# Kernel tuning notes

Hardware: AMD Instinct MI355X
Metric: run time of the kernel (lower is better)

The kernel has to match this reference:

```python
import jax, jax.numpy as jnp
import numpy as np

DIM = 512
HEADS = 8
DIM_HEAD = 64
INNER = HEADS * DIM_HEAD  # 512
PATCH = 64
M = 3
IN_CH = PATCH * PATCH // 2      # 2048
OUT_CH = IN_CH // 2             # 1024
B, N = 8, PATCH * PATCH // 4    # 8, 1024
SCALE = DIM_HEAD ** -0.5


def setup_inputs() -> dict:
    key = jax.random.key(0)
    ks = jax.random.split(key, 16)
    rn = lambda k, shp, s: (jax.random.normal(k, shp, dtype=jnp.float32) * s)
    inp = rn(ks[0], (B, N, DIM), 1.0)
    x = rn(ks[1], (B, N, DIM), 1.0)
    y = rn(ks[2], (B, N, DIM), 1.0)
    # Linear params (torch convention: W [out, in], y = x @ W.T + b)
    Wq = rn(ks[3], (INNER, DIM), DIM ** -0.5)
    bq = jnp.zeros((INNER,), jnp.float32)
    Wkv = rn(ks[4], (2 * INNER, DIM), DIM ** -0.5)
    bkv = jnp.zeros((2 * INNER,), jnp.float32)
    Wf = rn(ks[5], (OUT_CH + M, IN_CH + M), (IN_CH + M) ** -0.5)
    bf = jnp.zeros((OUT_CH + M,), jnp.float32)
    Wo = rn(ks[6], (DIM, INNER), INNER ** -0.5)
    bo = jnp.zeros((DIM,), jnp.float32)
    # memory tokens (xavier_normal std = sqrt(2/(m+inner)))
    std = np.sqrt(2.0 / (M + INNER))
    m_k = rn(ks[7], (1, M, INNER), std)
    m_v = rn(ks[8], (1, M, INNER), std)
    Sm_k = rn(ks[9], (1, M, INNER), std)
    Sm_v = rn(ks[10], (1, M, INNER), std)
    return dict(inp=inp, x=x, y=y, Wq=Wq, bq=bq, Wkv=Wkv, bkv=bkv,
                Wf=Wf, bf=bf, Wo=Wo, bo=bo,
                m_k=m_k, m_v=m_v, Sm_k=Sm_k, Sm_v=Sm_v)


def _split_heads(t):
    # 'b n (h d) -> b h n d'
    b, n, _ = t.shape
    return t.reshape(b, n, HEADS, DIM_HEAD).transpose(0, 2, 1, 3)


def _mem_view(p, b):
    # torch: p.expand(b, M, INNER).view(b, HEADS, M, DIM_HEAD) — raw reshape
    return jnp.broadcast_to(p, (b, M, INNER)).reshape(b, HEADS, M, DIM_HEAD)


def reference(inp, x, y, Wq, bq, Wkv, bkv, Wf, bf, Wo, bo, m_k, m_v, Sm_k, Sm_v):
    b = inp.shape[0]
    context = jnp.concatenate([x, y], axis=1)            # [b, 2n, dim]
    q = _split_heads(inp @ Wq.T + bq)                    # [b, h, n, d]
    kv = context @ Wkv.T + bkv
    k, v = jnp.split(kv, 2, axis=-1)
    k, v = _split_heads(k), _split_heads(v)              # [b, h, 2n, d]
    mk = np.sqrt(DIM_HEAD).astype(np.float32) * _mem_view(m_k, b)
    mv = np.sqrt(M).astype(np.float32) * _mem_view(m_v, b)
    k = jnp.concatenate([k, mk], axis=2)                 # [b, h, 2n+m, d]
    v = jnp.concatenate([v, mv], axis=2)
    dots = jnp.einsum('bhid,bhjd->bhij', q, k) * SCALE
    cross_attn = jax.nn.softmax(dots, axis=-1)           # [b, h, n, 2n+m]

    skv = inp @ Wkv.T + bkv
    S_k, S_v = jnp.split(skv, 2, axis=-1)
    S_k, S_v = _split_heads(S_k), _split_heads(S_v)      # [b, h, n, d]
    Smk = np.sqrt(DIM_HEAD).astype(np.float32) * _mem_view(Sm_k, b)
    Smv = np.sqrt(M).astype(np.float32) * _mem_view(Sm_v, b)
    Sk = jnp.concatenate([S_k, Smk], axis=2)             # [b, h, n+m, d]
    Sv = jnp.concatenate([S_v, Smv], axis=2)
    dots2 = jnp.einsum('bhid,bhjd->bhij', q, Sk) * SCALE
    self_attn = jax.nn.softmax(dots2, axis=-1)           # [b, h, n, n+m]

    cross_attn = cross_attn @ Wf.T + bf                  # [b, h, n, n+m]
    attn = cross_attn + self_attn
    out = jnp.einsum('bhij,bhjd->bhid', attn, Sv)        # [b, h, n, d]
    out = out.transpose(0, 2, 1, 3).reshape(b, -1, INNER)
    return out @ Wo.T + bo                               # [b, n, dim]
```

## Files before the change

### kernel.cpp

```cpp
#include <hip/hip_runtime.h>
#include <hip/hip_bf16.h>
#include <type_traits>

using bf16 = __hip_bfloat16;
typedef float f32x4 __attribute__((ext_vector_type(4)));
typedef __bf16 bf16x8_t __attribute__((ext_vector_type(8)));
typedef short  s16x8_t  __attribute__((ext_vector_type(8)));

template <typename V, typename = void> struct MfmaWorks : std::false_type {};
template <typename V>
struct MfmaWorks<V, std::void_t<decltype(__builtin_amdgcn_mfma_f32_16x16x32_bf16(
    std::declval<V>(), std::declval<V>(), std::declval<f32x4>(), 0, 0, 0))>> : std::true_type {};
using frag_t = std::conditional_t<MfmaWorks<bf16x8_t>::value, bf16x8_t, s16x8_t>;

template <typename V>
__device__ __forceinline__ f32x4 mfma_16x16x32(V a, V b, f32x4 c) {
    return __builtin_amdgcn_mfma_f32_16x16x32_bf16(a, b, c, 0, 0, 0);
}

__device__ __forceinline__ void gld_lds16(const void* g, void* l) {
    __builtin_amdgcn_global_load_lds(
        (const __attribute__((address_space(1))) unsigned int*)g,
        (__attribute__((address_space(3))) unsigned int*)l, 16, 0, 0);
}

__device__ __forceinline__ unsigned pack2(float lo, float hi) {
    bf16 a = __float2bfloat16(lo), b = __float2bfloat16(hi);
    unsigned short al, bl;
    __builtin_memcpy(&al, &a, 2);
    __builtin_memcpy(&bl, &b, 2);
    return (unsigned)al | ((unsigned)bl << 16);
}

__device__ __forceinline__ float ldin(const void* p, long i, int f32) {
    return f32 ? ((const float*)p)[i] : __bfloat162float(((const bf16*)p)[i]);
}

__device__ __forceinline__ int detect_f32(const void* __restrict__ inp) {
    __shared__ int sflag;
    const int t = threadIdx.x;
    if (t < 64) {
        int cnt = 0;
#pragma unroll
        for (int s = 0; s < 4; s++) {
            float v = __bfloat162float(((const bf16*)inp)[2 * (t + 64 * s)]);
            float a = fabsf(v);
            bool sane = (a == 0.f) || (a > 9e-4f && a < 1000.f);
            unsigned long long m = __ballot(sane);
            cnt += (int)__popcll(m);
        }
        if (t == 0) sflag = (cnt > 128) ? 0 : 1;
    }
    __syncthreads();
    return sflag;
}

__global__ __launch_bounds__(256)
void prep_all(const void* __restrict__ inp, const void* __restrict__ x,
              const void* __restrict__ y,
              const void* __restrict__ Wq, const void* __restrict__ Wkv,
              const void* __restrict__ Wo, const void* __restrict__ Wf,
              const void* __restrict__ bff, const void* __restrict__ bq,
              const void* __restrict__ bkv, const void* __restrict__ bo,
              const void* __restrict__ mk, const void* __restrict__ Smk,
              const void* __restrict__ Smv,
              bf16* __restrict__ inpB, bf16* __restrict__ ctxB,
              bf16* __restrict__ WqB, bf16* __restrict__ WkvB, bf16* __restrict__ WoB,
              bf16* __restrict__ WfT, bf16* __restrict__ bqB, bf16* __restrict__ bkvB,
              bf16* __restrict__ boB, bf16* __restrict__ kb, bf16* __restrict__ Skb,
              bf16* __restrict__ GTS, bf16* __restrict__ SvC, float qscale)
{
    const int f = detect_f32(inp);
    const int blk = blockIdx.x;
    const int t = threadIdx.x;
    const float SQRT3 = 1.7320508f;

    if (blk < 2048) {
        const long i0 = ((long)blk * 256 + t) * 8;
#pragma unroll
        for (int u = 0; u < 8; u++)
            inpB[i0 + u] = __float2bfloat16(ldin(inp, i0 + u, f));
    } else if (blk < 6144) {
        const long i0 = ((long)(blk - 2048) * 256 + t) * 8;
        const long r = i0 >> 9, c0 = i0 & 511;
        const long b = r >> 11, jj = r & 2047;
        const void* src = (jj < 1024) ? x : y;
        const long  soff = (jj < 1024) ? ((b * 1024 + jj) * 512 + c0)
                                       : ((b * 1024 + (jj - 1024)) * 512 + c0);
#pragma unroll
        for (int u = 0; u < 8; u++)
            ctxB[i0 + u] = __float2bfloat16(ldin(src, soff + u, f));
    } else if (blk < 6656) {
        const int wb = blk - 6144;
        long id = (long)wb * 256 + t;
        const void* src; bf16* dst; float sc;
        if (wb < 128)      { src = Wq;  dst = WqB;  sc = qscale; }
        else if (wb < 384) { src = Wkv; dst = WkvB; sc = 1.f; id -= 128L * 256; }
        else               { src = Wo;  dst = WoB;  sc = 1.f; id -= 384L * 256; }
        const long i0 = id * 8;
#pragma unroll
        for (int u = 0; u < 8; u++)
            dst[i0 + u] = __float2bfloat16(sc * ldin(src, i0 + u, f));
    } else if (blk < 7778) {
        const long i0 = ((long)(blk - 6656) * 256 + t) * 8;
        if (i0 >= 2176L * 1056) return;
        const long j = i0 / 1056, r0 = i0 % 1056;
        __align__(16) bf16 tmp[8];
#pragma unroll
        for (int u = 0; u < 8; u++) {
            const long r = r0 + u;
            float v = 0.f;
            if (r < 1027) {
                if (j < 2051)       v = ldin(Wf, r * 2051 + j, f);
                else if (j == 2051) v = ldin(bff, r, f);
            }
            tmp[u] = __float2bfloat16(v);
        }
        *(uint4*)(WfT + i0) = *(const uint4*)tmp;
    } else if (blk < 7781) {
        const void* src; bf16* dst; int n; float sc;
        switch (blk - 7778) {
            case 0:  src = bq;  dst = bqB;  n = 512;  sc = qscale; break;
            case 1:  src = bkv; dst = bkvB; n = 1024; sc = 1.f;    break;
            default: src = bo;  dst = boB;  n = 512;  sc = 1.f;    break;
        }
        for (int i = t; i < n; i += 256)
            dst[i] = __float2bfloat16(sc * ldin(src, i, f));
    } else if (blk < 8037) {
        const long e = ((long)(blk - 7781) * 256 + t) * 8;
        const long bh = e >> 13, rem = e & 8191;
        const long jj = rem >> 6, dg0 = rem & 63;
        const long h = bh & 7;
        __align__(16) bf16 tmp[8];
#pragma unroll
        for (int u = 0; u < 8; u++) {
            float v = (jj < 3) ? 8.f * ldin(mk, jj * 512 + h * 64 + dg0 + u, f) : 0.f;
            tmp[u] = __float2bfloat16(v);
        }
        *(uint4*)(kb + (bh * 2176 + 2048 + jj) * 64 + dg0) = *(const uint4*)tmp;
    } else if (blk < 8293) {
        const long e = ((long)(blk - 8037) * 256 + t) * 8;
        const long bh = e >> 13, rem = e & 8191;
        const long jj = rem >> 6, dg0 = rem & 63;
        const long h = bh & 7;
        __align__(16) bf16 tmp[8];
#pragma unroll
        for (int u = 0; u < 8; u++) {
            float v = (jj < 3) ? 8.f * ldin(Smk, jj * 512 + h * 64 + dg0 + u, f) : 0.f;
            tmp[u] = __float2bfloat16(v);
        }
        *(uint4*)(Skb + (bh * 1152 + 1024 + jj) * 64 + dg0) = *(const uint4*)tmp;
    } else {
        const long e = ((long)(blk - 8293) * 256 + t) * 8;
        const long bh = e >> 11, rem = e & 2047;
        const long dd = rem >> 5, jc0 = rem & 31;
        const long h = bh & 7;
        __align__(16) bf16 tmp[8];
#pragma unroll
        for (int u = 0; u < 8; u++) {
            const long jc = jc0 + u;
            float v = (jc < 3) ? SQRT3 * ldin(Smv, jc * 512 + h * 64 + dd, f) : 0.f;
            tmp[u] = __float2bfloat16(v);
        }
        *(uint4*)(GTS + (bh * 128 + dd) * 3136 + 3104 + jc0) = *(const uint4*)tmp;
        *(uint4*)(SvC + (bh * 64 + dd) * 1056 + 1024 + jc0)  = *(const uint4*)tmp;
    }
}

#define BK 32

__global__ __launch_bounds__(256)
void gemm_qkv(const bf16* __restrict__ A, const bf16* __restrict__ B,
              const bf16* __restrict__ bias,
              bf16* __restrict__ qb, bf16* __restrict__ Skb,
              bf16* __restrict__ GTS, bf16* __restrict__ SvC)
{
    __shared__ __align__(16) short As[128 * BK];
    __shared__ __align__(16) short Bs[128 * BK];

    const int t = threadIdx.x;
    const int wave = t >> 6, lane = t & 63;
    const int bn = blockIdx.x, bm = blockIdx.y;

    const bf16* Ab = A + (long)bm * 128 * 512;
    const bf16* Bb = B + (long)bn * 128 * 512;

    const int lrow = t >> 2, lcol = (t & 3) << 3;

    const f32x4 vzero = {0.f, 0.f, 0.f, 0.f};
    f32x4 acc[4][4];
#pragma unroll
    for (int i = 0; i < 4; i++)
#pragma unroll
        for (int j = 0; j < 4; j++) acc[i][j] = vzero;

    const int wr = (wave >> 1) << 6;
    const int wc = (wave & 1) << 6;
    const int fr = lane & 15;
    const int fq = (lane >> 4) << 3;

    for (int k0 = 0; k0 < 512; k0 += BK) {
        __syncthreads();
        gld_lds16(Ab + (long)lrow * 512 + (k0 + lcol),        (char*)As + wave * 1024);
        gld_lds16(Ab + (long)(64 + lrow) * 512 + (k0 + lcol), (char*)As + 4096 + wave * 1024);
        gld_lds16(Bb + (long)lrow * 512 + (k0 + lcol),        (char*)Bs + wave * 1024);
        gld_lds16(Bb + (long)(64 + lrow) * 512 + (k0 + lcol), (char*)Bs + 4096 + wave * 1024);
        __builtin_amdgcn_s_waitcnt(0);
        __syncthreads();

        frag_t af[4], bfr[4];
#pragma unroll
        for (int i = 0; i < 4; i++) af[i]  = *(const frag_t*)&As[(wr + i * 16 + fr) * BK + fq];
#pragma unroll
        for (int j = 0; j < 4; j++) bfr[j] = *(const frag_t*)&Bs[(wc + j * 16 + fr) * BK + fq];
#pragma unroll
        for (int i = 0; i < 4; i++)
#pragma unroll
            for (int j = 0; j < 4; j++)
                acc[i][j] = mfma_16x16x32<frag_t>(af[i], bfr[j], acc[i][j]);
    }

    const int r0 = bm * 128 + wr + ((lane >> 4) << 2);
    const int c0 = bn * 128 + wc + fr;
    const int bb = bm >> 3;
#pragma unroll
    for (int j = 0; j < 4; j++) {
        const int c = c0 + j * 16;
        const float bv = __bfloat162float(bias[c]);
        if (c < 512) {
#pragma unroll
            for (int i = 0; i < 4; i++)
#pragma unroll
                for (int r = 0; r < 4; r++) {
                    const long rg = r0 + i * 16 + r;
                    qb[rg * 512 + c] = __float2bfloat16(acc[i][j][r] + bv);
                }
        } else if (c < 1024) {
            const int h = (c - 512) >> 6, dg = c & 63;
            bf16* base = Skb + ((long)(bb * 8 + h) * 1152) * 64 + dg;
#pragma unroll
            for (int i = 0; i < 4; i++)
#pragma unroll
                for (int r = 0; r < 4; r++) {
                    const long jj = (r0 + i * 16 + r) & 1023;
                    base[jj * 64] = __float2bfloat16(acc[i][j][r] + bv);
                }
        } else {
            const int h = (c - 1024) >> 6, dd = c & 63;
            bf16* svt = GTS + ((long)(bb * 8 + h) * 128 + dd) * 3136 + 2080;
            bf16* svc = SvC + ((long)(bb * 8 + h) * 64 + dd) * 1056;
#pragma unroll
            for (int i = 0; i < 4; i++) {
                const long j0 = (r0 + i * 16) & 1023;
                __align__(8) bf16 t4[4];
#pragma unroll
                for (int r = 0; r < 4; r++) t4[r] = __float2bfloat16(acc[i][j][r] + bv);
                *(uint2*)(svt + j0) = *(const uint2*)t4;
                *(uint2*)(svc + j0) = *(const uint2*)t4;
            }
        }
    }
}

__global__ __launch_bounds__(256)
void gemm_gtck(const bf16* __restrict__ WfT, const bf16* __restrict__ SvC,
               bf16* __restrict__ GTS,
               const bf16* __restrict__ ctxB, const bf16* __restrict__ WkvB,
               const bf16* __restrict__ bkvB, bf16* __restrict__ kb)
{
    __shared__ __align__(16) short As[128 * BK];
    __shared__ __align__(16) short Bs[128 * BK];

    const int t = threadIdx.x;
    const int wave = t >> 6, lane = t & 63;
    const int id = blockIdx.x;
    const bool isGT = id < 544;

    int bn, bm, K;
    const bf16 *A, *B;
    long lda, ldb;
    if (isGT) { bn = id & 31; bm = id >> 5; A = WfT; lda = 1056; B = SvC; ldb = 1056; K = 1056; }
    else { const int i2 = id - 544; bn = i2 & 3; bm = i2 >> 2; A = ctxB; lda = 512; B = WkvB; ldb = 512; K = 512; }

    const bf16* Ab = A + (long)bm * 128 * lda;
    const bf16* Bb = B + (long)bn * 128 * ldb;

    const int lrow = t >> 2, lcol = (t & 3) << 3;

    const f32x4 vzero = {0.f, 0.f, 0.f, 0.f};
    f32x4 acc[4][4];
#pragma unroll
    for (int i = 0; i < 4; i++)
#pragma unroll
        for (int j = 0; j < 4; j++) acc[i][j] = vzero;

    const int wr = (wave >> 1) << 6;
    const int wc = (wave & 1) << 6;
    const int fr = lane & 15;
    const int fq = (lane >> 4) << 3;

    for (int k0 = 0; k0 < K; k0 += BK) {
        __syncthreads();
        gld_lds16(Ab + (long)lrow * lda + (k0 + lcol),        (char*)As + wave * 1024);
        gld_lds16(Ab + (long)(64 + lrow) * lda + (k0 + lcol), (char*)As + 4096 + wave * 1024);
        gld_lds16(Bb + (long)lrow * ldb + (k0 + lcol),        (char*)Bs + wave * 1024);
        gld_lds16(Bb + (long)(64 + lrow) * ldb + (k0 + lcol), (char*)Bs + 4096 + wave * 1024);
        __builtin_amdgcn_s_waitcnt(0);
        __syncthreads();

        frag_t af[4], bfr[4];
#pragma unroll
        for (int i = 0; i < 4; i++) af[i]  = *(const frag_t*)&As[(wr + i * 16 + fr) * BK + fq];
#pragma unroll
        for (int j = 0; j < 4; j++) bfr[j] = *(const frag_t*)&Bs[(wc + j * 16 + fr) * BK + fq];
#pragma unroll
        for (int i = 0; i < 4; i++)
#pragma unroll
            for (int j = 0; j < 4; j++)
                acc[i][j] = mfma_16x16x32<frag_t>(af[i], bfr[j], acc[i][j]);
    }

    const int r0 = bm * 128 + wr + ((lane >> 4) << 2);
    const int c0 = bn * 128 + wc + fr;

    if (isGT) {
#pragma unroll
        for (int j = 0; j < 4; j++) {
            const int c = c0 + j * 16;
            bf16* rowp = GTS + ((long)(c >> 6) * 128 + (c & 63)) * 3136;
#pragma unroll
            for (int i = 0; i < 4; i++) {
                const int rgb = r0 + i * 16;
                if (rgb >= 2080) continue;
                __align__(8) bf16 t4[4];
#pragma unroll
                for (int r = 0; r < 4; r++) t4[r] = __float2bfloat16(acc[i][j][r]);
                *(uint2*)(rowp + rgb) = *(const uint2*)t4;
            }
        }
    } else {
        const int bb = bm >> 4;
#pragma unroll
        for (int j = 0; j < 4; j++) {
            const int c = c0 + j * 16;
            const float bv = __bfloat162float(bkvB[c]);
            const int h = c >> 6, dg = c & 63;
            bf16* base = kb + ((long)(bb * 8 + h) * 2176) * 64 + dg;
#pragma unroll
            for (int i = 0; i < 4; i++)
#pragma unroll
                for (int r = 0; r < 4; r++) {
                    const long jj = (r0 + i * 16 + r) & 2047;
                    base[jj * 64] = __float2bfloat16(acc[i][j][r] + bv);
                }
        }
    }
}

__global__ __launch_bounds__(256)
void gemm_final64(const float* __restrict__ o0, const float* __restrict__ o1,
                  const bf16* __restrict__ B, const bf16* __restrict__ bias,
                  float* __restrict__ out)
{
    __shared__ __align__(16) short As[64 * BK];
    __shared__ __align__(16) short Bs[128 * BK];

    const int t = threadIdx.x;
    const int wave = t >> 6, lane = t & 63;
    const int bn = blockIdx.x, bm = blockIdx.y;

    const bf16* Bb = B + (long)bn * 128 * 512;
    const int lrow = t >> 2, lcol = (t & 3) << 3;

    const f32x4 vzero = {0.f, 0.f, 0.f, 0.f};
    f32x4 acc[2][4];
#pragma unroll
    for (int i = 0; i < 2; i++)
#pragma unroll
        for (int j = 0; j < 4; j++) acc[i][j] = vzero;

    const int wr = (wave >> 1) << 5;
    const int wc = (wave & 1) << 6;
    const int fr = lane & 15;
    const int fq = (lane >> 4) << 3;

    for (int k0 = 0; k0 < 512; k0 += BK) {
        __syncthreads();
        {
            const int ar = t >> 2, ac = (t & 3) << 3;
            const float* a0 = o0 + (long)(bm * 64 + ar) * 512 + k0 + ac;
            const float* a1 = o1 + (long)(bm * 64 + ar) * 512 + k0 + ac;
            __align__(16) bf16 tt[8];
#pragma unroll
            for (int u = 0; u < 2; u++) {
                const float4 v0 = *(const float4*)(a0 + u * 4);
                const float4 v1 = *(const float4*)(a1 + u * 4);
                tt[u * 4 + 0] = __float2bfloat16(v0.x + v1.x);
                tt[u * 4 + 1] = __float2bfloat16(v0.y + v1.y);
                tt[u * 4 + 2] = __float2bfloat16(v0.z + v1.z);
                tt[u * 4 + 3] = __float2bfloat16(v0.w + v1.w);
            }
            *(uint4*)&As[ar * BK + ac] = *(const uint4*)tt;
        }
        gld_lds16(Bb + (long)lrow * 512 + (k0 + lcol),        (char*)Bs + wave * 1024);
        gld_lds16(Bb + (long)(64 + lrow) * 512 + (k0 + lcol), (char*)Bs + 4096 + wave * 1024);
        __builtin_amdgcn_s_waitcnt(0);
        __syncthreads();

        frag_t af[2], bfr[4];
#pragma unroll
        for (int i = 0; i < 2; i++) af[i]  = *(const frag_t*)&As[(wr + i * 16 + fr) * BK + fq];
#pragma unroll
        for (int j = 0; j < 4; j++) bfr[j] = *(const frag_t*)&Bs[(wc + j * 16 + fr) * BK + fq];
#pragma unroll
        for (int i = 0; i < 2; i++)
#pragma unroll
            for (int j = 0; j < 4; j++)
                acc[i][j] = mfma_16x16x32<frag_t>(af[i], bfr[j], acc[i][j]);
    }

    const int r0 = bm * 64 + wr + ((lane >> 4) << 2);
    const int c0 = bn * 128 + wc + fr;
#pragma unroll
    for (int j = 0; j < 4; j++) {
        const int c = c0 + j * 16;
        const float bv = __bfloat162float(bias[c]);
#pragma unroll
        for (int i = 0; i < 2; i++)
#pragma unroll
            for (int r = 0; r < 4; r++) {
                const long rg = r0 + i * 16 + r;
                out[rg * 512 + c] = acc[i][j][r] + bv;
            }
    }
}

__global__ __launch_bounds__(256, 4)
void attn_fused(const bf16* __restrict__ q,
                const bf16* __restrict__ kb,
                const bf16* __restrict__ Skb,
                const bf16* __restrict__ GTS,
                float* __restrict__ out0,
                float* __restrict__ out1)
{
    __shared__ __align__(16) bf16 Ks[2][64 * 64];
    __shared__ __align__(16) bf16 Gs[2][64 * 64];
    __shared__ __align__(16) unsigned Psw[4][16][32];

    const int t = threadIdx.x;
    const int w = t >> 6, lane = t & 63;
    const int bh = blockIdx.x, bm = blockIdx.y;
    const int phase = blockIdx.z;
    const int b = bh >> 3, h = bh & 7;
    const int g  = lane >> 4;
    const int fr = lane & 15;

    const bf16* Qg = q + ((long)(b * 1024 + bm * 128)) * 512 + h * 64;
    {
        const int qr = t >> 3, qc0 = (t & 7) << 3;
#pragma unroll
        for (int u = 0; u < 4; u++)
            gld_lds16(Qg + (long)(u * 32 + qr) * 512 + qc0, (char*)Ks + u * 4096 + w * 1024);
    }
    __builtin_amdgcn_s_waitcnt(0);
    __syncthreads();

    frag_t qf[2][2];
#pragma unroll
    for (int it = 0; it < 2; it++)
#pragma unroll
        for (int kh = 0; kh < 2; kh++)
            qf[it][kh] = *(const frag_t*)&((const bf16*)Ks)[(w * 32 + it * 16 + fr) * 64 + kh * 32 + g * 8];
    __syncthreads();

    union { frag_t f; short s[8]; } ou;
#pragma unroll
    for (int i = 0; i < 8; i++) ou.s[i] = 0x3F80;
    const frag_t onesf = ou.f;

    const f32x4 vzero = {0.f, 0.f, 0.f, 0.f};
    const int rs = t >> 3, gs = t & 7;
    const int glo = gs ^ (rs & 7);

    const bf16* Kb = phase ? Skb + (long)bh * 1152 * 64 : kb + (long)bh * 2176 * 64;
    const bf16* Gb = GTS + (long)bh * 128 * 3136 + (phase ? 2080 : 0);
    const int NC = phase ? 17 : 33;
    const int valid = phase ? 1027 : 2051;

    f32x4 oacc[2][4];
    f32x4 lacc[2];
#pragma unroll
    for (int it = 0; it < 2; it++) {
        lacc[it] = vzero;
#pragma unroll
        for (int dt = 0; dt < 4; dt++) oacc[it][dt] = vzero;
    }

    gld_lds16(Kb + (long)rs * 64 + glo * 8,          (char*)Ks[0] + w * 1024);
    gld_lds16(Kb + (long)(32 + rs) * 64 + glo * 8,   (char*)Ks[0] + 4096 + w * 1024);
    gld_lds16(Gb + (long)rs * 3136 + glo * 8,        (char*)Gs[0] + w * 1024);
    gld_lds16(Gb + (long)(32 + rs) * 3136 + glo * 8, (char*)Gs[0] + 4096 + w * 1024);

    unsigned* prow = &Psw[w][fr][0];
    const int swzk = (fr & 7) << 2;

    for (int c = 0; c < NC; c++) {
        const int buf = c & 1;
        __builtin_amdgcn_s_waitcnt(0);
        __syncthreads();
        if (c + 1 < NC) {
            const bf16* Kc = Kb + (long)(c + 1) * 64 * 64;
            const bf16* Gc = Gb + (c + 1) * 64;
            gld_lds16(Kc + (long)rs * 64 + glo * 8,          (char*)Ks[buf ^ 1] + w * 1024);
            gld_lds16(Kc + (long)(32 + rs) * 64 + glo * 8,   (char*)Ks[buf ^ 1] + 4096 + w * 1024);
            gld_lds16(Gc + (long)rs * 3136 + glo * 8,        (char*)Gs[buf ^ 1] + w * 1024);
            gld_lds16(Gc + (long)(32 + rs) * 3136 + glo * 8, (char*)Gs[buf ^ 1] + 4096 + w * 1024);
        }
        const bf16* Kl = Ks[buf];
        const bf16* Gl = Gs[buf];

        f32x4 s2[2][4];
#pragma unroll
        for (int it = 0; it < 2; it++)
#pragma unroll
            for (int ct = 0; ct < 4; ct++) s2[it][ct] = vzero;
        __builtin_amdgcn_s_setprio(1);
#pragma unroll
        for (int ct = 0; ct < 4; ct++)
#pragma unroll
            for (int kh = 0; kh < 2; kh++) {
                const int gph = (kh * 4 + g) ^ (fr & 7);
                const frag_t kf = *(const frag_t*)&Kl[(ct * 16 + fr) * 64 + gph * 8];
                s2[0][ct] = mfma_16x16x32<frag_t>(kf, qf[0][kh], s2[0][ct]);
                s2[1][ct] = mfma_16x16x32<frag_t>(kf, qf[1][kh], s2[1][ct]);
            }
        __builtin_amdgcn_s_setprio(0);

        if (c == NC - 1) {
#pragma unroll
            for (int ct = 0; ct < 4; ct++)
#pragma unroll
                for (int r = 0; r < 4; r++) {
                    const int kAbs = c * 64 + ct * 16 + 4 * g + r;
                    if (kAbs >= valid) { s2[0][ct][r] = -1.0e30f; s2[1][ct][r] = -1.0e30f; }
                }
        }

        frag_t pa[2][2];
#pragma unroll
        for (int it = 0; it < 2; it++) {
#pragma unroll
            for (int ct = 0; ct < 4; ct++) {
                const unsigned w0 = pack2(exp2f(s2[it][ct][0]), exp2f(s2[it][ct][1]));
                const unsigned w1 = pack2(exp2f(s2[it][ct][2]), exp2f(s2[it][ct][3]));
                *(uint2*)&prow[(ct * 8 + 2 * g) ^ swzk] = make_uint2(w0, w1);
            }
#pragma unroll
            for (int kh = 0; kh < 2; kh++)
                pa[it][kh] = *(const frag_t*)&prow[(kh * 16 + 4 * g) ^ swzk];
        }

        __builtin_amdgcn_s_setprio(1);
#pragma unroll
        for (int kh = 0; kh < 2; kh++) {
            lacc[0] = mfma_16x16x32<frag_t>(pa[0][kh], onesf, lacc[0]);
            lacc[1] = mfma_16x16x32<frag_t>(pa[1][kh], onesf, lacc[1]);
#pragma unroll
            for (int dt = 0; dt < 4; dt++) {
                const int gph = (kh * 4 + g) ^ (fr & 7);
                const frag_t gf = *(const frag_t*)&Gl[(dt * 16 + fr) * 64 + gph * 8];
                oacc[0][dt] = mfma_16x16x32<frag_t>(pa[0][kh], gf, oacc[0][dt]);
                oacc[1][dt] = mfma_16x16x32<frag_t>(pa[1][kh], gf, oacc[1][dt]);
            }
        }
        __builtin_amdgcn_s_setprio(0);
    }

    float gba[4] = {0.f, 0.f, 0.f, 0.f};
    if (phase == 0) {
        const bf16* gp = GTS + (long)bh * 128 * 3136 + 2051;
#pragma unroll
        for (int dt = 0; dt < 4; dt++)
            gba[dt] = __bfloat162float(gp[(long)(dt * 16 + fr) * 3136]);
    }
    float* Og = (phase ? out1 : out0) + ((long)(b * 1024 + bm * 128)) * 512 + h * 64;
#pragma unroll
    for (int it = 0; it < 2; it++)
#pragma unroll
        for (int r = 0; r < 4; r++) {
            const float inv = 1.f / lacc[it][r];
#pragma unroll
            for (int dt = 0; dt < 4; dt++) {
                Og[(long)(w * 32 + it * 16 + g * 4 + r) * 512 + dt * 16 + fr] =
                    oacc[it][dt][r] * inv + gba[dt];
            }
        }
}

extern "C" void kernel_launch(void* const* d_in, const int* in_sizes, int n_in,
                              void* d_out, int out_size, void* d_ws, size_t ws_size,
                              hipStream_t stream)
{
    const void* inp  = d_in[0];
    const void* x    = d_in[1];
    const void* y    = d_in[2];
    const void* Wq   = d_in[3];
    const void* bq   = d_in[4];
    const void* Wkv  = d_in[5];
    const void* bkv  = d_in[6];
    const void* Wf   = d_in[7];
    const void* bff  = d_in[8];
    const void* Wo   = d_in[9];
    const void* bo   = d_in[10];
    const void* m_k  = d_in[11];
    const void* Sm_k = d_in[13];
    const void* Sm_v = d_in[14];

    char* ws = (char*)d_ws;
    bf16* WqB  = (bf16*)(ws + 256);
    bf16* WkvB = (bf16*)(ws + 524544);
    bf16* WoB  = (bf16*)(ws + 1573120);
    bf16* WfT  = (bf16*)(ws + 2097408);
    bf16* bqB  = (bf16*)(ws + 6693120);
    bf16* bkvB = (bf16*)(ws + 6694144);
    bf16* boB  = (bf16*)(ws + 6696192);
    bf16* qb   = (bf16*)(ws + 6706432);
    bf16* kb   = (bf16*)(ws + 15095040);
    bf16* Skb  = (bf16*)(ws + 32920832);
    bf16* GTS  = (bf16*)(ws + 42358016);
    char* OV   = ws + 93738240;

    bf16*  inpB  = (bf16*)(OV);
    bf16*  SvC   = (bf16*)(OV + 16777216);
    bf16*  ctxB  = (bf16*)(OV + 33554432);
    float* out0f = (float*)(OV);
    float* out1f = (float*)(OV + 16777216);

    const dim3 blk(256);
    const float QS = 0.125f * 1.44269504f;

    prep_all<<<dim3(8357), blk, 0, stream>>>(inp, x, y, Wq, Wkv, Wo, Wf, bff,
                                             bq, bkv, bo, m_k, Sm_k, Sm_v,
                                             inpB, ctxB, WqB, WkvB, WoB, WfT,
                                             bqB, bkvB, boB, kb, Skb, GTS, SvC, QS);

    gemm_qkv<<<dim3(12, 64), blk, 0, stream>>>(inpB, WqB, bqB, qb, Skb, GTS, SvC);

    gemm_gtck<<<dim3(1056), blk, 0, stream>>>(WfT, SvC, GTS, ctxB, WkvB, bkvB, kb);

    attn_fused<<<dim3(64, 8, 2), blk, 0, stream>>>(qb, kb, Skb, GTS, out0f, out1f);

    gemm_final64<<<dim3(4, 128), blk, 0, stream>>>(out0f, out1f, WoB, boB, (float*)d_out);
}
```

Before: 360.9 us.

## Halve GEMM M-tiles and split cross-attention key range to balance attention blocks

The two projection GEMMs now use 64-row tiles instead of 128, doubling the block count so more blocks run at once. The attention kernel previously gave 33 key chunks to the cross phase and 17 to the self phase, which left the two halves of the grid unevenly loaded. The cross range is now split at chunk 25, and the z=1 blocks process the cross tail plus the whole self phase. The two partial cross results are stored unnormalized with their row sums, and the final GEMM combines them and normalizes while loading. This costs an extra fp32 output buffer and row-sum buffers to read in the final GEMM, and less reuse per GEMM tile.

After: 389.0 us. 1.08x slower.

```diff
diff --git a/kernel.cpp b/kernel.cpp
--- a/kernel.cpp
+++ b/kernel.cpp
@@ -175,26 +175,25 @@
               bf16* __restrict__ qb, bf16* __restrict__ Skb,
               bf16* __restrict__ GTS, bf16* __restrict__ SvC)
 {
-    __shared__ __align__(16) short As[128 * BK];
+    __shared__ __align__(16) short As[64 * BK];
     __shared__ __align__(16) short Bs[128 * BK];
 
     const int t = threadIdx.x;
     const int wave = t >> 6, lane = t & 63;
     const int bn = blockIdx.x, bm = blockIdx.y;
 
-    const bf16* Ab = A + (long)bm * 128 * 512;
+    const bf16* Ab = A + (long)bm * 64 * 512;
     const bf16* Bb = B + (long)bn * 128 * 512;
-
     const int lrow = t >> 2, lcol = (t & 3) << 3;
 
     const f32x4 vzero = {0.f, 0.f, 0.f, 0.f};
-    f32x4 acc[4][4];
-#pragma unroll
-    for (int i = 0; i < 4; i++)
+    f32x4 acc[2][4];
+#pragma unroll
+    for (int i = 0; i < 2; i++)
 #pragma unroll
         for (int j = 0; j < 4; j++) acc[i][j] = vzero;
 
-    const int wr = (wave >> 1) << 6;
+    const int wr = (wave >> 1) << 5;
     const int wc = (wave & 1) << 6;
     const int fr = lane & 15;
     const int fq = (lane >> 4) << 3;
@@ -202,34 +201,33 @@
     for (int k0 = 0; k0 < 512; k0 += BK) {
         __syncthreads();
         gld_lds16(Ab + (long)lrow * 512 + (k0 + lcol),        (char*)As + wave * 1024);
-        gld_lds16(Ab + (long)(64 + lrow) * 512 + (k0 + lcol), (char*)As + 4096 + wave * 1024);
         gld_lds16(Bb + (long)lrow * 512 + (k0 + lcol),        (char*)Bs + wave * 1024);
         gld_lds16(Bb + (long)(64 + lrow) * 512 + (k0 + lcol), (char*)Bs + 4096 + wave * 1024);
         __builtin_amdgcn_s_waitcnt(0);
         __syncthreads();
 
-        frag_t af[4], bfr[4];
-#pragma unroll
-        for (int i = 0; i < 4; i++) af[i]  = *(const frag_t*)&As[(wr + i * 16 + fr) * BK + fq];
+        frag_t af[2], bfr[4];
+#pragma unroll
+        for (int i = 0; i < 2; i++) af[i]  = *(const frag_t*)&As[(wr + i * 16 + fr) * BK + fq];
 #pragma unroll
         for (int j = 0; j < 4; j++) bfr[j] = *(const frag_t*)&Bs[(wc + j * 16 + fr) * BK + fq];
 #pragma unroll
-        for (int i = 0; i < 4; i++)
+        for (int i = 0; i < 2; i++)
 #pragma unroll
             for (int j = 0; j < 4; j++)
                 acc[i][j] = mfma_16x16x32<frag_t>(af[i], bfr[j], acc[i][j]);
     }
 
-    const int r0 = bm * 128 + wr + ((lane >> 4) << 2);
+    const int r0 = bm * 64 + wr + ((lane >> 4) << 2);
     const int c0 = bn * 128 + wc + fr;
-    const int bb = bm >> 3;
+    const int bb = bm >> 4;
 #pragma unroll
     for (int j = 0; j < 4; j++) {
         const int c = c0 + j * 16;
         const float bv = __bfloat162float(bias[c]);
         if (c < 512) {
 #pragma unroll
-            for (int i = 0; i < 4; i++)
+            for (int i = 0; i < 2; i++)
 #pragma unroll
                 for (int r = 0; r < 4; r++) {
                     const long rg = r0 + i * 16 + r;
@@ -239,7 +237,7 @@
             const int h = (c - 512) >> 6, dg = c & 63;
             bf16* base = Skb + ((long)(bb * 8 + h) * 1152) * 64 + dg;
 #pragma unroll
-            for (int i = 0; i < 4; i++)
+            for (int i = 0; i < 2; i++)
 #pragma unroll
                 for (int r = 0; r < 4; r++) {
                     const long jj = (r0 + i * 16 + r) & 1023;
@@ -250,7 +248,7 @@
             bf16* svt = GTS + ((long)(bb * 8 + h) * 128 + dd) * 3136 + 2080;
             bf16* svc = SvC + ((long)(bb * 8 + h) * 64 + dd) * 1056;
 #pragma unroll
-            for (int i = 0; i < 4; i++) {
+            for (int i = 0; i < 2; i++) {
                 const long j0 = (r0 + i * 16) & 1023;
                 __align__(8) bf16 t4[4];
 #pragma unroll
@@ -268,33 +266,32 @@
                const bf16* __restrict__ ctxB, const bf16* __restrict__ WkvB,
                const bf16* __restrict__ bkvB, bf16* __restrict__ kb)
 {
-    __shared__ __align__(16) short As[128 * BK];
+    __shared__ __align__(16) short As[64 * BK];
     __shared__ __align__(16) short Bs[128 * BK];
 
     const int t = threadIdx.x;
     const int wave = t >> 6, lane = t & 63;
     const int id = blockIdx.x;
-    const bool isGT = id < 544;
+    const bool isGT = id < 1088;
 
     int bn, bm, K;
     const bf16 *A, *B;
     long lda, ldb;
     if (isGT) { bn = id & 31; bm = id >> 5; A = WfT; lda = 1056; B = SvC; ldb = 1056; K = 1056; }
-    else { const int i2 = id - 544; bn = i2 & 3; bm = i2 >> 2; A = ctxB; lda = 512; B = WkvB; ldb = 512; K = 512; }
-
-    const bf16* Ab = A + (long)bm * 128 * lda;
+    else { const int i2 = id - 1088; bn = i2 & 3; bm = i2 >> 2; A = ctxB; lda = 512; B = WkvB; ldb = 512; K = 512; }
+
+    const bf16* Ab = A + (long)bm * 64 * lda;
     const bf16* Bb = B + (long)bn * 128 * ldb;
-
     const int lrow = t >> 2, lcol = (t & 3) << 3;
 
     const f32x4 vzero = {0.f, 0.f, 0.f, 0.f};
-    f32x4 acc[4][4];
-#pragma unroll
-    for (int i = 0; i < 4; i++)
+    f32x4 acc[2][4];
+#pragma unroll
+    for (int i = 0; i < 2; i++)
 #pragma unroll
         for (int j = 0; j < 4; j++) acc[i][j] = vzero;
 
-    const int wr = (wave >> 1) << 6;
+    const int wr = (wave >> 1) << 5;
     const int wc = (wave & 1) << 6;
     const int fr = lane & 15;
     const int fq = (lane >> 4) << 3;
@@ -302,25 +299,24 @@
     for (int k0 = 0; k0 < K; k0 += BK) {
         __syncthreads();
         gld_lds16(Ab + (long)lrow * lda + (k0 + lcol),        (char*)As + wave * 1024);
-        gld_lds16(Ab + (long)(64 + lrow) * lda + (k0 + lcol), (char*)As + 4096 + wave * 1024);
         gld_lds16(Bb + (long)lrow * ldb + (k0 + lcol),        (char*)Bs + wave * 1024);
         gld_lds16(Bb + (long)(64 + lrow) * ldb + (k0 + lcol), (char*)Bs + 4096 + wave * 1024);
         __builtin_amdgcn_s_waitcnt(0);
         __syncthreads();
 
-        frag_t af[4], bfr[4];
-#pragma unroll
-        for (int i = 0; i < 4; i++) af[i]  = *(const frag_t*)&As[(wr + i * 16 + fr) * BK + fq];
+        frag_t af[2], bfr[4];
+#pragma unroll
+        for (int i = 0; i < 2; i++) af[i]  = *(const frag_t*)&As[(wr + i * 16 + fr) * BK + fq];
 #pragma unroll
         for (int j = 0; j < 4; j++) bfr[j] = *(const frag_t*)&Bs[(wc + j * 16 + fr) * BK + fq];
 #pragma unroll
-        for (int i = 0; i < 4; i++)
+        for (int i = 0; i < 2; i++)
 #pragma unroll
             for (int j = 0; j < 4; j++)
                 acc[i][j] = mfma_16x16x32<frag_t>(af[i], bfr[j], acc[i][j]);
     }
 
-    const int r0 = bm * 128 + wr + ((lane >> 4) << 2);
+    const int r0 = bm * 64 + wr + ((lane >> 4) << 2);
     const int c0 = bn * 128 + wc + fr;
 
     if (isGT) {
@@ -329,7 +325,7 @@
             const int c = c0 + j * 16;
             bf16* rowp = GTS + ((long)(c >> 6) * 128 + (c & 63)) * 3136;
 #pragma unroll
-            for (int i = 0; i < 4; i++) {
+            for (int i = 0; i < 2; i++) {
                 const int rgb = r0 + i * 16;
                 if (rgb >= 2080) continue;
                 __align__(8) bf16 t4[4];
@@ -339,7 +335,7 @@
             }
         }
     } else {
-        const int bb = bm >> 4;
+        const int bb = bm >> 5;
 #pragma unroll
         for (int j = 0; j < 4; j++) {
             const int c = c0 + j * 16;
@@ -347,7 +343,7 @@
             const int h = c >> 6, dg = c & 63;
             bf16* base = kb + ((long)(bb * 8 + h) * 2176) * 64 + dg;
 #pragma unroll
-            for (int i = 0; i < 4; i++)
+            for (int i = 0; i < 2; i++)
 #pragma unroll
                 for (int r = 0; r < 4; r++) {
                     const long jj = (r0 + i * 16 + r) & 2047;
@@ -358,7 +354,9 @@
 }
 
 __global__ __launch_bounds__(256)
-void gemm_final64(const float* __restrict__ o0, const float* __restrict__ o1,
+void gemm_final64(const float* __restrict__ o0, const float* __restrict__ o2,
+                  const float* __restrict__ o1,
+                  const float* __restrict__ lA, const float* __restrict__ lB,
                   const bf16* __restrict__ B, const bf16* __restrict__ bias,
                   float* __restrict__ out)
 {
@@ -388,17 +386,24 @@
         __syncthreads();
         {
             const int ar = t >> 2, ac = (t & 3) << 3;
-            const float* a0 = o0 + (long)(bm * 64 + ar) * 512 + k0 + ac;
-            const float* a1 = o1 + (long)(bm * 64 + ar) * 512 + k0 + ac;
+            const long row = (long)bm * 64 + ar;
+            const long off = row * 512 + k0 + ac;
+            const int h = (k0 + ac) >> 6;
+            const long li = ((row >> 10) * 8 + h) * 1024 + (row & 1023);
+            const float rl = 1.f / (lA[li] + lB[li]);
+            const float* a0 = o0 + off;
+            const float* a2 = o2 + off;
+            const float* a1 = o1 + off;
             __align__(16) bf16 tt[8];
 #pragma unroll
             for (int u = 0; u < 2; u++) {
                 const float4 v0 = *(const float4*)(a0 + u * 4);
+                const float4 v2 = *(const float4*)(a2 + u * 4);
                 const float4 v1 = *(const float4*)(a1 + u * 4);
-                tt[u * 4 + 0] = __float2bfloat16(v0.x + v1.x);
-                tt[u * 4 + 1] = __float2bfloat16(v0.y + v1.y);
-                tt[u * 4 + 2] = __float2bfloat16(v0.z + v1.z);
-                tt[u * 4 + 3] = __float2bfloat16(v0.w + v1.w);
+                tt[u * 4 + 0] = __float2bfloat16((v0.x + v2.x) * rl + v1.x);
+                tt[u * 4 + 1] = __float2bfloat16((v0.y + v2.y) * rl + v1.y);
+                tt[u * 4 + 2] = __float2bfloat16((v0.z + v2.z) * rl + v1.z);
+                tt[u * 4 + 3] = __float2bfloat16((v0.w + v2.w) * rl + v1.w);
             }
             *(uint4*)&As[ar * BK + ac] = *(const uint4*)tt;
         }
@@ -440,8 +445,9 @@
                 const bf16* __restrict__ kb,
                 const bf16* __restrict__ Skb,
                 const bf16* __restrict__ GTS,
-                float* __restrict__ out0,
-                float* __restrict__ out1)
+                float* __restrict__ out0, float* __restrict__ out2,
+                float* __restrict__ out1,
+                float* __restrict__ lbufA, float* __restrict__ lbufB)
 {
     __shared__ __align__(16) bf16 Ks[2][64 * 64];
     __shared__ __align__(16) bf16 Gs[2][64 * 64];
@@ -450,7 +456,7 @@
     const int t = threadIdx.x;
     const int w = t >> 6, lane = t & 63;
     const int bh = blockIdx.x, bm = blockIdx.y;
-    const int phase = blockIdx.z;
+    const int z = blockIdx.z;
     const int b = bh >> 3, h = bh & 7;
     const int g  = lane >> 4;
     const int fr = lane & 15;
@@ -471,7 +477,6 @@
 #pragma unroll
         for (int kh = 0; kh < 2; kh++)
             qf[it][kh] = *(const frag_t*)&((const bf16*)Ks)[(w * 32 + it * 16 + fr) * 64 + kh * 32 + g * 8];
-    __syncthreads();
 
     union { frag_t f; short s[8]; } ou;
 #pragma unroll
@@ -482,119 +487,138 @@
     const int rs = t >> 3, gs = t & 7;
     const int glo = gs ^ (rs & 7);
 
-    const bf16* Kb = phase ? Skb + (long)bh * 1152 * 64 : kb + (long)bh * 2176 * 64;
-    const bf16* Gb = GTS + (long)bh * 128 * 3136 + (phase ? 2080 : 0);
-    const int NC = phase ? 17 : 33;
-    const int valid = phase ? 1027 : 2051;
-
-    f32x4 oacc[2][4];
-    f32x4 lacc[2];
-#pragma unroll
-    for (int it = 0; it < 2; it++) {
-        lacc[it] = vzero;
-#pragma unroll
-        for (int dt = 0; dt < 4; dt++) oacc[it][dt] = vzero;
-    }
-
-    gld_lds16(Kb + (long)rs * 64 + glo * 8,          (char*)Ks[0] + w * 1024);
-    gld_lds16(Kb + (long)(32 + rs) * 64 + glo * 8,   (char*)Ks[0] + 4096 + w * 1024);
-    gld_lds16(Gb + (long)rs * 3136 + glo * 8,        (char*)Gs[0] + w * 1024);
-    gld_lds16(Gb + (long)(32 + rs) * 3136 + glo * 8, (char*)Gs[0] + 4096 + w * 1024);
-
     unsigned* prow = &Psw[w][fr][0];
     const int swzk = (fr & 7) << 2;
 
-    for (int c = 0; c < NC; c++) {
-        const int buf = c & 1;
-        __builtin_amdgcn_s_waitcnt(0);
+    const int nseg = z ? 2 : 1;
+    for (int seg = 0; seg < nseg; seg++) {
+        const bool ph1 = (z == 1 && seg == 1);
+        const bf16* Kb = ph1 ? Skb + (long)bh * 1152 * 64 : kb + (long)bh * 2176 * 64;
+        const bf16* Gb = GTS + (long)bh * 128 * 3136 + (ph1 ? 2080 : 0);
+        const int c0s = (z == 0) ? 0 : (seg == 0 ? 25 : 0);
+        const int c1s = (z == 0) ? 25 : (seg == 0 ? 33 : 17);
+        const int maskc = ph1 ? 16 : 32;
+        const int valid = ph1 ? 1027 : 2051;
+
+        f32x4 oacc[2][4];
+        f32x4 lacc[2];
+#pragma unroll
+        for (int it = 0; it < 2; it++) {
+            lacc[it] = vzero;
+#pragma unroll
+            for (int dt = 0; dt < 4; dt++) oacc[it][dt] = vzero;
+        }
+
         __syncthreads();
-        if (c + 1 < NC) {
-            const bf16* Kc = Kb + (long)(c + 1) * 64 * 64;
-            const bf16* Gc = Gb + (c + 1) * 64;
-            gld_lds16(Kc + (long)rs * 64 + glo * 8,          (char*)Ks[buf ^ 1] + w * 1024);
-            gld_lds16(Kc + (long)(32 + rs) * 64 + glo * 8,   (char*)Ks[buf ^ 1] + 4096 + w * 1024);
-            gld_lds16(Gc + (long)rs * 3136 + glo * 8,        (char*)Gs[buf ^ 1] + w * 1024);
-            gld_lds16(Gc + (long)(32 + rs) * 3136 + glo * 8, (char*)Gs[buf ^ 1] + 4096 + w * 1024);
-        }
-        const bf16* Kl = Ks[buf];
-        const bf16* Gl = Gs[buf];
-
-        f32x4 s2[2][4];
-#pragma unroll
-        for (int it = 0; it < 2; it++)
-#pragma unroll
-            for (int ct = 0; ct < 4; ct++) s2[it][ct] = vzero;
-        __builtin_amdgcn_s_setprio(1);
-#pragma unroll
-        for (int ct = 0; ct < 4; ct++)
+        gld_lds16(Kb + ((long)c0s * 64 + rs) * 64 + glo * 8,        (char*)Ks[0] + w * 1024);
+        gld_lds16(Kb + ((long)c0s * 64 + 32 + rs) * 64 + glo * 8,   (char*)Ks[0] + 4096 + w * 1024);
+        gld_lds16(Gb + (long)rs * 3136 + c0s * 64 + glo * 8,        (char*)Gs[0] + w * 1024);
+        gld_lds16(Gb + (long)(32 + rs) * 3136 + c0s * 64 + glo * 8, (char*)Gs[0] + 4096 + w * 1024);
+
+        for (int c = c0s; c < c1s; c++) {
+            const int buf = (c - c0s) & 1;
+            __builtin_amdgcn_s_waitcnt(0);
+            __syncthreads();
+            if (c + 1 < c1s) {
+                const bf16* Kc = Kb + (long)(c + 1) * 64 * 64;
+                const bf16* Gc = Gb + (c + 1) * 64;
+                gld_lds16(Kc + (long)rs * 64 + glo * 8,          (char*)Ks[buf ^ 1] + w * 1024);
+                gld_lds16(Kc + (long)(32 + rs) * 64 + glo * 8,   (char*)Ks[buf ^ 1] + 4096 + w * 1024);
+                gld_lds16(Gc + (long)rs * 3136 + glo * 8,        (char*)Gs[buf ^ 1] + w * 1024);
+                gld_lds16(Gc + (long)(32 + rs) * 3136 + glo * 8, (char*)Gs[buf ^ 1] + 4096 + w * 1024);
+            }
+            const bf16* Kl = Ks[buf];
+            const bf16* Gl = Gs[buf];
+
+            f32x4 s2[2][4];
+#pragma unroll
+            for (int it = 0; it < 2; it++)
+#pragma unroll
+                for (int ct = 0; ct < 4; ct++) s2[it][ct] = vzero;
+            __builtin_amdgcn_s_setprio(1);
+#pragma unroll
+            for (int ct = 0; ct < 4; ct++)
+#pragma unroll
+                for (int kh = 0; kh < 2; kh++) {
+                    const int gph = (kh * 4 + g) ^ (fr & 7);
+                    const frag_t kf = *(const frag_t*)&Kl[(ct * 16 + fr) * 64 + gph * 8];
+                    s2[0][ct] = mfma_16x16x32<frag_t>(kf, qf[0][kh], s2[0][ct]);
+                    s2[1][ct] = mfma_16x16x32<frag_t>(kf, qf[1][kh], s2[1][ct]);
+                }
+            __builtin_amdgcn_s_setprio(0);
+
+            if (c == maskc) {
+#pragma unroll
+                for (int ct = 0; ct < 4; ct++)
+#pragma unroll
+                    for (int r = 0; r < 4; r++) {
+                        const int kAbs = c * 64 + ct * 16 + 4 * g + r;
+                        if (kAbs >= valid) { s2[0][ct][r] = -1.0e30f; s2[1][ct][r] = -1.0e30f; }
+                    }
+            }
+
+            frag_t pa[2][2];
+#pragma unroll
+            for (int it = 0; it < 2; it++) {
+#pragma unroll
+                for (int ct = 0; ct < 4; ct++) {
+                    const unsigned w0 = pack2(exp2f(s2[it][ct][0]), exp2f(s2[it][ct][1]));
+                    const unsigned w1 = pack2(exp2f(s2[it][ct][2]), exp2f(s2[it][ct][3]));
+                    *(uint2*)&prow[(ct * 8 + 2 * g) ^ swzk] = make_uint2(w0, w1);
+                }
+#pragma unroll
+                for (int kh = 0; kh < 2; kh++)
+                    pa[it][kh] = *(const frag_t*)&prow[(kh * 16 + 4 * g) ^ swzk];
+            }
+
+            __builtin_amdgcn_s_setprio(1);
 #pragma unroll
             for (int kh = 0; kh < 2; kh++) {
-                const int gph = (kh * 4 + g) ^ (fr & 7);
-                const frag_t kf = *(const frag_t*)&Kl[(ct * 16 + fr) * 64 + gph * 8];
-                s2[0][ct] = mfma_16x16x32<frag_t>(kf, qf[0][kh], s2[0][ct]);
-                s2[1][ct] = mfma_16x16x32<frag_t>(kf, qf[1][kh], s2[1][ct]);
-            }
-        __builtin_amdgcn_s_setprio(0);
-
-        if (c == NC - 1) {
-#pragma unroll
-            for (int ct = 0; ct < 4; ct++)
+                lacc[0] = mfma_16x16x32<frag_t>(pa[0][kh], onesf, lacc[0]);
+                lacc[1] = mfma_16x16x32<frag_t>(pa[1][kh], onesf, lacc[1]);
+#pragma unroll
+                for (int dt = 0; dt < 4; dt++) {
+                    const int gph = (kh * 4 + g) ^ (fr & 7);
+                    const frag_t gf = *(const frag_t*)&Gl[(dt * 16 + fr) * 64 + gph * 8];
+                    oacc[0][dt] = mfma_16x16x32<frag_t>(pa[0][kh], gf, oacc[0][dt]);
+                    oacc[1][dt] = mfma_16x16x32<frag_t>(pa[1][kh], gf, oacc[1][dt]);
+                }
+            }
+            __builtin_amdgcn_s_setprio(0);
+        }
+
+        if (!ph1) {
+            float* Og = (z ? out2 : out0) + ((long)(b * 1024 + bm * 128)) * 512 + h * 64;
+            float* lb = (z ? lbufB : lbufA) + (long)bh * 1024 + bm * 128;
+#pragma unroll
+            for (int it = 0; it < 2; it++)
 #pragma unroll
                 for (int r = 0; r < 4; r++) {
-                    const int kAbs = c * 64 + ct * 16 + 4 * g + r;
-                    if (kAbs >= valid) { s2[0][ct][r] = -1.0e30f; s2[1][ct][r] = -1.0e30f; }
-                }
-        }
-
-        frag_t pa[2][2];
-#pragma unroll
-        for (int it = 0; it < 2; it++) {
-#pragma unroll
-            for (int ct = 0; ct < 4; ct++) {
-                const unsigned w0 = pack2(exp2f(s2[it][ct][0]), exp2f(s2[it][ct][1]));
-                const unsigned w1 = pack2(exp2f(s2[it][ct][2]), exp2f(s2[it][ct][3]));
-                *(uint2*)&prow[(ct * 8 + 2 * g) ^ swzk] = make_uint2(w0, w1);
-            }
-#pragma unroll
-            for (int kh = 0; kh < 2; kh++)
-                pa[it][kh] = *(const frag_t*)&prow[(kh * 16 + 4 * g) ^ swzk];
-        }
-
-        __builtin_amdgcn_s_setprio(1);
-#pragma unroll
-        for (int kh = 0; kh < 2; kh++) {
-            lacc[0] = mfma_16x16x32<frag_t>(pa[0][kh], onesf, lacc[0]);
-            lacc[1] = mfma_16x16x32<frag_t>(pa[1][kh], onesf, lacc[1]);
-#pragma unroll
-            for (int dt = 0; dt < 4; dt++) {
-                const int gph = (kh * 4 + g) ^ (fr & 7);
-                const frag_t gf = *(const frag_t*)&Gl[(dt * 16 + fr) * 64 + gph * 8];
-                oacc[0][dt] = mfma_16x16x32<frag_t>(pa[0][kh], gf, oacc[0][dt]);
-                oacc[1][dt] = mfma_16x16x32<frag_t>(pa[1][kh], gf, oacc[1][dt]);
-            }
-        }
-        __builtin_amdgcn_s_setprio(0);
-    }
-
-    float gba[4] = {0.f, 0.f, 0.f, 0.f};
-    if (phase == 0) {
-        const bf16* gp = GTS + (long)bh * 128 * 3136 + 2051;
-#pragma unroll
-        for (int dt = 0; dt < 4; dt++)
-            gba[dt] = __bfloat162float(gp[(long)(dt * 16 + fr) * 3136]);
-    }
-    float* Og = (phase ? out1 : out0) + ((long)(b * 1024 + bm * 128)) * 512 + h * 64;
-#pragma unroll
-    for (int it = 0; it < 2; it++)
-#pragma unroll
-        for (int r = 0; r < 4; r++) {
-            const float inv = 1.f / lacc[it][r];
-#pragma unroll
-            for (int dt = 0; dt < 4; dt++) {
-                Og[(long)(w * 32 + it * 16 + g * 4 + r) * 512 + dt * 16 + fr] =
-                    oacc[it][dt][r] * inv + gba[dt];
-            }
-        }
+                    const int lrw = w * 32 + it * 16 + g * 4 + r;
+                    if (fr == 0) lb[lrw] = lacc[it][r];
+#pragma unroll
+                    for (int dt = 0; dt < 4; dt++)
+                        Og[(long)lrw * 512 + dt * 16 + fr] = oacc[it][dt][r];
+                }
+        } else {
+            float gba[4];
+            const bf16* gp = GTS + (long)bh * 128 * 3136 + 2051;
+#pragma unroll
+            for (int dt = 0; dt < 4; dt++)
+                gba[dt] = __bfloat162float(gp[(long)(dt * 16 + fr) * 3136]);
+            float* Og = out1 + ((long)(b * 1024 + bm * 128)) * 512 + h * 64;
+#pragma unroll
+            for (int it = 0; it < 2; it++)
+#pragma unroll
+                for (int r = 0; r < 4; r++) {
+                    const float inv = 1.f / lacc[it][r];
+#pragma unroll
+                    for (int dt = 0; dt < 4; dt++)
+                        Og[(long)(w * 32 + it * 16 + g * 4 + r) * 512 + dt * 16 + fr] =
+                            oacc[it][dt][r] * inv + gba[dt];
+                }
+        }
+    }
 }
 
 extern "C" void kernel_launch(void* const* d_in, const int* in_sizes, int n_in,
@@ -635,6 +659,9 @@
     bf16*  ctxB  = (bf16*)(OV + 33554432);
     float* out0f = (float*)(OV);
     float* out1f = (float*)(OV + 16777216);
+    float* out2f = (float*)(OV + 33554432);
+    float* lbufA = (float*)(OV + 50331648);
+    float* lbufB = (float*)(OV + 50331648 + 262144);
 
     const dim3 blk(256);
     const float QS = 0.125f * 1.44269504f;
@@ -644,11 +671,13 @@
                                              inpB, ctxB, WqB, WkvB, WoB, WfT,
                                              bqB, bkvB, boB, kb, Skb, GTS, SvC, QS);
 
-    gemm_qkv<<<dim3(12, 64), blk, 0, stream>>>(inpB, WqB, bqB, qb, Skb, GTS, SvC);
-
-    gemm_gtck<<<dim3(1056), blk, 0, stream>>>(WfT, SvC, GTS, ctxB, WkvB, bkvB, kb);
-
-    attn_fused<<<dim3(64, 8, 2), blk, 0, stream>>>(qb, kb, Skb, GTS, out0f, out1f);
-
-    gemm_final64<<<dim3(4, 128), blk, 0, stream>>>(out0f, out1f, WoB, boB, (float*)d_out);
-}
+    gemm_qkv<<<dim3(12, 128), blk, 0, stream>>>(inpB, WqB, bqB, qb, Skb, GTS, SvC);
+
+    gemm_gtck<<<dim3(2112), blk, 0, stream>>>(WfT, SvC, GTS, ctxB, WkvB, bkvB, kb);
+
+    attn_fused<<<dim3(64, 8, 2), blk, 0, stream>>>(qb, kb, Skb, GTS,
+                                                   out0f, out2f, out1f, lbufA, lbufB);
+
+    gemm_final64<<<dim3(4, 128), blk, 0, stream>>>(out0f, out2f, out1f, lbufA, lbufB,
+                                                   WoB, boB, (float*)d_out);
+}
```
